# Kernel tuning notes

Measured on AMD Instinct MI355X. Metric: run time of the kernel, lower is better.

The kernel has to match this reference:

```python
import jax, jax.numpy as jnp
import numpy as np

N_HEADS = 16
D_KV = 64
TRIL_DIAG = -999999  # faithful to torch.tril(scores, diagonal=-999999)


def setup_inputs() -> dict:
    key = jax.random.key(0)
    ks = jax.random.split(key, 5)
    B, S, D = 2, 2048, 1024
    inner = N_HEADS * D_KV
    return {
        "hidden_states": jax.random.normal(ks[0], (B, S, D), dtype=jnp.float32),
        "Wq": jax.random.normal(ks[1], (inner, D), dtype=jnp.float32) * 0.02,
        "Wk": jax.random.normal(ks[2], (inner, D), dtype=jnp.float32) * 0.02,
        "Wv": jax.random.normal(ks[3], (inner, D), dtype=jnp.float32) * 0.02,
        "Wo": jax.random.normal(ks[4], (D, inner), dtype=jnp.float32) * 0.02,
    }


def reference(hidden_states, Wq, Wk, Wv, Wo):
    B, S, D = hidden_states.shape

    def shape(x):  # [B,S,inner] -> [B,H,S,Dk]
        return x.reshape(B, S, N_HEADS, D_KV).transpose(0, 2, 1, 3)

    q = shape(hidden_states @ Wq.T)
    k = shape(hidden_states @ Wk.T)
    v = shape(hidden_states @ Wv.T)

    scores = jnp.einsum("bhqd,bhkd->bhqk", q, k)  # no 1/sqrt(d) scaling, as in source
    scores = jnp.tril(scores, k=TRIL_DIAG)  # zeroes everything for S < 999999 (faithful)
    attn = jax.nn.softmax(scores.astype(jnp.float32), axis=-1).astype(scores.dtype)
    # dropout is identity at inference
    ctx = jnp.einsum("bhqk,bhkd->bhqd", attn, v)
    ctx = ctx.transpose(0, 2, 1, 3).reshape(B, S, N_HEADS * D_KV)
    return ctx @ Wo.T
```

## Files before the change

kernel.cpp:

```cpp
#include <hip/hip_runtime.h>

#define BB 2
#define SS 2048
#define DD 1024
#define INNER 1024
#define NCHUNK 64
#define ROWS_PER_CHUNK (SS / NCHUNK)

__global__ void colsum_kernel(const float* __restrict__ h, float* __restrict__ hbar) {
    int b = blockIdx.x / NCHUNK;
    int chunk = blockIdx.x % NCHUNK;
    int t = threadIdx.x;
    const float4* hp = reinterpret_cast<const float4*>(h + (size_t)b * SS * DD);
    float4 acc = make_float4(0.f, 0.f, 0.f, 0.f);
    int s0 = chunk * ROWS_PER_CHUNK;
    #pragma unroll 4
    for (int s = s0; s < s0 + ROWS_PER_CHUNK; ++s) {
        float4 v = hp[(size_t)s * (DD / 4) + t];
        acc.x += v.x; acc.y += v.y; acc.z += v.z; acc.w += v.w;
    }
    float* dst = hbar + b * DD + t * 4;
    atomicAdd(dst + 0, acc.x);
    atomicAdd(dst + 1, acc.y);
    atomicAdd(dst + 2, acc.z);
    atomicAdd(dst + 3, acc.w);
}

__global__ void matvec_kernel(const float* __restrict__ W, const float* __restrict__ x,
                              float* __restrict__ y, float scale) {
    int wave = (blockIdx.x * blockDim.x + threadIdx.x) >> 6;
    int lane = threadIdx.x & 63;
    int b = wave / INNER;
    int i = wave % INNER;
    const float4* Wp = reinterpret_cast<const float4*>(W + (size_t)i * 1024);
    const float4* xp = reinterpret_cast<const float4*>(x + b * 1024);
    float sum = 0.f;
    #pragma unroll
    for (int k4 = lane; k4 < 256; k4 += 64) {
        float4 w = Wp[k4];
        float4 xv = xp[k4];
        sum += w.x * xv.x + w.y * xv.y + w.z * xv.z + w.w * xv.w;
    }
    #pragma unroll
    for (int off = 32; off > 0; off >>= 1) sum += __shfl_down(sum, off);
    if (lane == 0) y[wave] = sum * scale;
}

__global__ void bcast_kernel(const float* __restrict__ row, float* __restrict__ out) {
    const float4* r4 = reinterpret_cast<const float4*>(row);
    float4* o4 = reinterpret_cast<float4*>(out);
    const int total4 = BB * SS * (DD / 4);
    for (int i = blockIdx.x * blockDim.x + threadIdx.x; i < total4;
         i += gridDim.x * blockDim.x) {
        int d4 = i & (DD / 4 - 1);
        int b = i >> 19;
        o4[i] = r4[b * (DD / 4) + d4];
    }
}

extern "C" void kernel_launch(void* const* d_in, const int* in_sizes, int n_in,
                              void* d_out, int out_size, void* d_ws, size_t ws_size,
                              hipStream_t stream) {
    const float* h  = (const float*)d_in[0];
    const float* Wv = (const float*)d_in[3];
    const float* Wo = (const float*)d_in[4];
    float* out = (float*)d_out;

    float* hbar  = (float*)d_ws;
    float* vmean = hbar + BB * DD;
    float* orow  = vmean + BB * INNER;

    hipMemsetAsync(hbar, 0, BB * DD * sizeof(float), stream);
    colsum_kernel<<<BB * NCHUNK, 256, 0, stream>>>(h, hbar);
    matvec_kernel<<<512, 256, 0, stream>>>(Wv, hbar, vmean, 1.0f / (float)SS);
    matvec_kernel<<<512, 256, 0, stream>>>(Wo, vmean, orow, 1.0f);
    bcast_kernel<<<2048, 256, 0, stream>>>(orow, out);
}
```

Measured before the change: 96.36 us.

## Fuse colsum, matvecs and broadcast into one cooperative kernel with grid syncs

Replaces the memset plus four separate launches with a single cooperative kernel that runs column sums, the two matvecs and the output broadcast as phases separated by grid.sync. Atomic accumulation is replaced by per-block partial sums that are reduced in a second phase. The aim is to remove launch overhead and the gaps between kernels. In exchange it adds four grid-wide barriers, limits the grid to 256 blocks, and the reduction phase runs on only 2048 threads.

Measured after the change: 209.4 us. 117% more time.

```diff
diff --git a/kernel.cpp b/kernel.cpp
--- a/kernel.cpp
+++ b/kernel.cpp
@@ -1,60 +1,109 @@
 #include <hip/hip_runtime.h>
+#include <hip/hip_cooperative_groups.h>
+
+namespace cg = cooperative_groups;
 
 #define BB 2
 #define SS 2048
 #define DD 1024
-#define INNER 1024
-#define NCHUNK 64
-#define ROWS_PER_CHUNK (SS / NCHUNK)
+#define NBLK 256
+#define NTHR 256
+#define ROWS_PER_BLK 16
 
-__global__ void colsum_kernel(const float* __restrict__ h, float* __restrict__ hbar) {
-    int b = blockIdx.x / NCHUNK;
-    int chunk = blockIdx.x % NCHUNK;
-    int t = threadIdx.x;
-    const float4* hp = reinterpret_cast<const float4*>(h + (size_t)b * SS * DD);
-    float4 acc = make_float4(0.f, 0.f, 0.f, 0.f);
-    int s0 = chunk * ROWS_PER_CHUNK;
-    #pragma unroll 4
-    for (int s = s0; s < s0 + ROWS_PER_CHUNK; ++s) {
-        float4 v = hp[(size_t)s * (DD / 4) + t];
-        acc.x += v.x; acc.y += v.y; acc.z += v.z; acc.w += v.w;
+__global__ void __launch_bounds__(NTHR, 1)
+fused_kernel(const float* __restrict__ h, const float* __restrict__ Wv,
+             const float* __restrict__ Wo, float* __restrict__ out,
+             float* __restrict__ ws) {
+    cg::grid_group grid = cg::this_grid();
+
+    float* partial = ws;
+    float* hbar    = ws + NBLK * DD;
+    float* vmean   = hbar + BB * DD;
+    float* orow    = vmean + BB * DD;
+
+    const int bid = blockIdx.x;
+    const int tid = threadIdx.x;
+    const int gtid = bid * NTHR + tid;
+    const int lane = tid & 63;
+    const int wave = gtid >> 6;
+
+    {
+        const float4* hp = reinterpret_cast<const float4*>(h);
+        float4 acc = make_float4(0.f, 0.f, 0.f, 0.f);
+        int r0 = bid * ROWS_PER_BLK;
+        #pragma unroll 4
+        for (int r = r0; r < r0 + ROWS_PER_BLK; ++r) {
+            float4 v = hp[(size_t)r * (DD / 4) + tid];
+            acc.x += v.x; acc.y += v.y; acc.z += v.z; acc.w += v.w;
+        }
+        reinterpret_cast<float4*>(partial)[bid * (DD / 4) + tid] = acc;
     }
-    float* dst = hbar + b * DD + t * 4;
-    atomicAdd(dst + 0, acc.x);
-    atomicAdd(dst + 1, acc.y);
-    atomicAdd(dst + 2, acc.z);
-    atomicAdd(dst + 3, acc.w);
-}
+    grid.sync();
 
-__global__ void matvec_kernel(const float* __restrict__ W, const float* __restrict__ x,
-                              float* __restrict__ y, float scale) {
-    int wave = (blockIdx.x * blockDim.x + threadIdx.x) >> 6;
-    int lane = threadIdx.x & 63;
-    int b = wave / INNER;
-    int i = wave % INNER;
-    const float4* Wp = reinterpret_cast<const float4*>(W + (size_t)i * 1024);
-    const float4* xp = reinterpret_cast<const float4*>(x + b * 1024);
-    float sum = 0.f;
-    #pragma unroll
-    for (int k4 = lane; k4 < 256; k4 += 64) {
-        float4 w = Wp[k4];
-        float4 xv = xp[k4];
-        sum += w.x * xv.x + w.y * xv.y + w.z * xv.z + w.w * xv.w;
+    if (gtid < BB * DD) {
+        int b = gtid >> 10;
+        int d = gtid & (DD - 1);
+        float s = 0.f;
+        #pragma unroll 8
+        for (int j = 0; j < 128; ++j)
+            s += partial[(size_t)(b * 128 + j) * DD + d];
+        hbar[gtid] = s;
     }
-    #pragma unroll
-    for (int off = 32; off > 0; off >>= 1) sum += __shfl_down(sum, off);
-    if (lane == 0) y[wave] = sum * scale;
-}
+    grid.sync();
 
-__global__ void bcast_kernel(const float* __restrict__ row, float* __restrict__ out) {
-    const float4* r4 = reinterpret_cast<const float4*>(row);
-    float4* o4 = reinterpret_cast<float4*>(out);
-    const int total4 = BB * SS * (DD / 4);
-    for (int i = blockIdx.x * blockDim.x + threadIdx.x; i < total4;
-         i += gridDim.x * blockDim.x) {
-        int d4 = i & (DD / 4 - 1);
-        int b = i >> 19;
-        o4[i] = r4[b * (DD / 4) + d4];
+    {
+        #pragma unroll
+        for (int rep = 0; rep < 2; ++rep) {
+            int o = wave + rep * 1024;
+            int b = o >> 10;
+            int i = o & (DD - 1);
+            const float4* Wp = reinterpret_cast<const float4*>(Wv + (size_t)i * DD);
+            const float4* xp = reinterpret_cast<const float4*>(hbar + b * DD);
+            float sum = 0.f;
+            #pragma unroll
+            for (int k4 = lane; k4 < DD / 4; k4 += 64) {
+                float4 w = Wp[k4];
+                float4 x = xp[k4];
+                sum += w.x * x.x + w.y * x.y + w.z * x.z + w.w * x.w;
+            }
+            #pragma unroll
+            for (int off = 32; off > 0; off >>= 1) sum += __shfl_down(sum, off);
+            if (lane == 0) vmean[o] = sum * (1.0f / (float)SS);
+        }
+    }
+    grid.sync();
+
+    {
+        #pragma unroll
+        for (int rep = 0; rep < 2; ++rep) {
+            int o = wave + rep * 1024;
+            int b = o >> 10;
+            int i = o & (DD - 1);
+            const float4* Wp = reinterpret_cast<const float4*>(Wo + (size_t)i * DD);
+            const float4* xp = reinterpret_cast<const float4*>(vmean + b * DD);
+            float sum = 0.f;
+            #pragma unroll
+            for (int k4 = lane; k4 < DD / 4; k4 += 64) {
+                float4 w = Wp[k4];
+                float4 x = xp[k4];
+                sum += w.x * x.x + w.y * x.y + w.z * x.z + w.w * x.w;
+            }
+            #pragma unroll
+            for (int off = 32; off > 0; off >>= 1) sum += __shfl_down(sum, off);
+            if (lane == 0) orow[o] = sum;
+        }
+    }
+    grid.sync();
+
+    {
+        const float4* r4 = reinterpret_cast<const float4*>(orow);
+        float4* o4 = reinterpret_cast<float4*>(out);
+        const int total4 = BB * SS * (DD / 4);
+        for (int i = gtid; i < total4; i += NBLK * NTHR) {
+            int d4 = i & (DD / 4 - 1);
+            int b = i >> 19;
+            o4[i] = r4[b * (DD / 4) + d4];
+        }
     }
 }
 
@@ -65,14 +114,9 @@
     const float* Wv = (const float*)d_in[3];
     const float* Wo = (const float*)d_in[4];
     float* out = (float*)d_out;
+    float* ws  = (float*)d_ws;
 
-    float* hbar  = (float*)d_ws;
-    float* vmean = hbar + BB * DD;
-    float* orow  = vmean + BB * INNER;
-
-    hipMemsetAsync(hbar, 0, BB * DD * sizeof(float), stream);
-    colsum_kernel<<<BB * NCHUNK, 256, 0, stream>>>(h, hbar);
-    matvec_kernel<<<512, 256, 0, stream>>>(Wv, hbar, vmean, 1.0f / (float)SS);
-    matvec_kernel<<<512, 256, 0, stream>>>(Wo, vmean, orow, 1.0f);
-    bcast_kernel<<<2048, 256, 0, stream>>>(orow, out);
+    void* args[] = { (void*)&h, (void*)&Wv, (void*)&Wo, (void*)&out, (void*)&ws };
+    hipLaunchCooperativeKernel((const void*)fused_kernel, dim3(NBLK), dim3(NTHR),
+                               args, 0, stream);
 }
```

## Replace atomics with partial sums and fuse matvecs with reduction and broadcast

Applied to the files above, without the earlier changes.

Column sums now go to per-chunk partial buffers instead of atomics, removing the memset. The first matvec reduces the partials itself into shared memory. The second matvec is fused with the output broadcast, so each block computes its own slice of the output row and writes its tile. This removes two launches but makes every block recompute the partial reduction and the Wo rows, so far more redundant reads go through L2.

After: 115.5 us. +19.9%, slower.

```diff
diff --git a/kernel.cpp b/kernel.cpp
--- a/kernel.cpp
+++ b/kernel.cpp
@@ -3,58 +3,114 @@
 #define BB 2
 #define SS 2048
 #define DD 1024
-#define INNER 1024
-#define NCHUNK 64
-#define ROWS_PER_CHUNK (SS / NCHUNK)
 
-__global__ void colsum_kernel(const float* __restrict__ h, float* __restrict__ hbar) {
-    int b = blockIdx.x / NCHUNK;
-    int chunk = blockIdx.x % NCHUNK;
+__global__ void colsum_kernel(const float* __restrict__ h, float* __restrict__ partial) {
+    int bid = blockIdx.x;
+    int b = bid >> 6;
+    int chunk = bid & 63;
     int t = threadIdx.x;
-    const float4* hp = reinterpret_cast<const float4*>(h + (size_t)b * SS * DD);
+    const float4* hp = reinterpret_cast<const float4*>(h) + (size_t)b * SS * (DD / 4);
     float4 acc = make_float4(0.f, 0.f, 0.f, 0.f);
-    int s0 = chunk * ROWS_PER_CHUNK;
+    int s0 = chunk * 32;
     #pragma unroll 4
-    for (int s = s0; s < s0 + ROWS_PER_CHUNK; ++s) {
+    for (int s = s0; s < s0 + 32; ++s) {
         float4 v = hp[(size_t)s * (DD / 4) + t];
         acc.x += v.x; acc.y += v.y; acc.z += v.z; acc.w += v.w;
     }
-    float* dst = hbar + b * DD + t * 4;
-    atomicAdd(dst + 0, acc.x);
-    atomicAdd(dst + 1, acc.y);
-    atomicAdd(dst + 2, acc.z);
-    atomicAdd(dst + 3, acc.w);
+    reinterpret_cast<float4*>(partial)[(size_t)bid * (DD / 4) + t] = acc;
 }
 
-__global__ void matvec_kernel(const float* __restrict__ W, const float* __restrict__ x,
-                              float* __restrict__ y, float scale) {
-    int wave = (blockIdx.x * blockDim.x + threadIdx.x) >> 6;
-    int lane = threadIdx.x & 63;
-    int b = wave / INNER;
-    int i = wave % INNER;
-    const float4* Wp = reinterpret_cast<const float4*>(W + (size_t)i * 1024);
-    const float4* xp = reinterpret_cast<const float4*>(x + b * 1024);
-    float sum = 0.f;
+__global__ void matvec1_kernel(const float* __restrict__ Wv, const float* __restrict__ partial,
+                               float* __restrict__ vmean) {
+    __shared__ float4 hbar4[2 * (DD / 4)];
+    int t = threadIdx.x;
+    const float4* p4 = reinterpret_cast<const float4*>(partial);
+    float4 a0 = make_float4(0.f, 0.f, 0.f, 0.f);
+    float4 a1 = make_float4(0.f, 0.f, 0.f, 0.f);
+    #pragma unroll 8
+    for (int j = 0; j < 64; ++j) {
+        float4 v0 = p4[(size_t)j * (DD / 4) + t];
+        float4 v1 = p4[(size_t)(64 + j) * (DD / 4) + t];
+        a0.x += v0.x; a0.y += v0.y; a0.z += v0.z; a0.w += v0.w;
+        a1.x += v1.x; a1.y += v1.y; a1.z += v1.z; a1.w += v1.w;
+    }
+    hbar4[t] = a0;
+    hbar4[256 + t] = a1;
+    __syncthreads();
+
+    int wv = t >> 6, lane = t & 63;
+    int i0 = blockIdx.x * 32;
     #pragma unroll
-    for (int k4 = lane; k4 < 256; k4 += 64) {
-        float4 w = Wp[k4];
-        float4 xv = xp[k4];
-        sum += w.x * xv.x + w.y * xv.y + w.z * xv.z + w.w * xv.w;
+    for (int r = 0; r < 16; ++r) {
+        int ol = wv * 16 + r;
+        int il = ol >> 1, b = ol & 1;
+        int i = i0 + il;
+        const float4* Wp = reinterpret_cast<const float4*>(Wv) + (size_t)i * (DD / 4);
+        float sum = 0.f;
+        #pragma unroll
+        for (int p = 0; p < 4; ++p) {
+            float4 w = Wp[lane + p * 64];
+            float4 x = hbar4[b * 256 + lane + p * 64];
+            sum += w.x * x.x + w.y * x.y + w.z * x.z + w.w * x.w;
+        }
+        #pragma unroll
+        for (int off = 32; off > 0; off >>= 1) sum += __shfl_down(sum, off);
+        if (lane == 0) vmean[b * DD + i] = sum * (1.0f / (float)SS);
     }
-    #pragma unroll
-    for (int off = 32; off > 0; off >>= 1) sum += __shfl_down(sum, off);
-    if (lane == 0) y[wave] = sum * scale;
 }
 
-__global__ void bcast_kernel(const float* __restrict__ row, float* __restrict__ out) {
-    const float4* r4 = reinterpret_cast<const float4*>(row);
+__global__ void matvec2_bcast_kernel(const float* __restrict__ Wo, const float* __restrict__ vmean,
+                                     float* __restrict__ out) {
+    __shared__ float4 vm4[2 * (DD / 4)];
+    __shared__ float4 orow4[2 * 32];
+    int t = threadIdx.x, wv = t >> 6, lane = t & 63;
+    int bid = blockIdx.x;
+    int sc = bid >> 3, ic = bid & 7;
+    int i0 = ic * 128, s0 = sc * 128;
+
+    const float4* vg = reinterpret_cast<const float4*>(vmean);
+    vm4[t] = vg[t];
+    vm4[256 + t] = vg[256 + t];
+    __syncthreads();
+
+    float4 x0[4], x1[4];
+    #pragma unroll
+    for (int p = 0; p < 4; ++p) {
+        x0[p] = vm4[lane + p * 64];
+        x1[p] = vm4[256 + lane + p * 64];
+    }
+
+    float* orow = reinterpret_cast<float*>(orow4);
+    #pragma unroll 4
+    for (int r = 0; r < 32; ++r) {
+        int il = wv * 32 + r;
+        int i = i0 + il;
+        const float4* Wp = reinterpret_cast<const float4*>(Wo) + (size_t)i * (DD / 4);
+        float sb0 = 0.f, sb1 = 0.f;
+        #pragma unroll
+        for (int p = 0; p < 4; ++p) {
+            float4 w = Wp[lane + p * 64];
+            sb0 += w.x * x0[p].x + w.y * x0[p].y + w.z * x0[p].z + w.w * x0[p].w;
+            sb1 += w.x * x1[p].x + w.y * x1[p].y + w.z * x1[p].z + w.w * x1[p].w;
+        }
+        #pragma unroll
+        for (int off = 32; off > 0; off >>= 1) {
+            sb0 += __shfl_down(sb0, off);
+            sb1 += __shfl_down(sb1, off);
+        }
+        if (lane == 0) {
+            orow[0 * 128 + il] = sb0;
+            orow[1 * 128 + il] = sb1;
+        }
+    }
+    __syncthreads();
+
     float4* o4 = reinterpret_cast<float4*>(out);
-    const int total4 = BB * SS * (DD / 4);
-    for (int i = blockIdx.x * blockDim.x + threadIdx.x; i < total4;
-         i += gridDim.x * blockDim.x) {
-        int d4 = i & (DD / 4 - 1);
-        int b = i >> 19;
-        o4[i] = r4[b * (DD / 4) + d4];
+    for (int j = t; j < 8192; j += 256) {
+        int q4 = j & 31;
+        int s = (j >> 5) & 127;
+        int b = j >> 12;
+        o4[((size_t)(b * SS + s0 + s)) * (DD / 4) + ic * 32 + q4] = orow4[b * 32 + q4];
     }
 }
 
@@ -66,13 +122,10 @@
     const float* Wo = (const float*)d_in[4];
     float* out = (float*)d_out;
 
-    float* hbar  = (float*)d_ws;
-    float* vmean = hbar + BB * DD;
-    float* orow  = vmean + BB * INNER;
+    float* partial = (float*)d_ws;
+    float* vmean   = partial + 128 * DD;
 
-    hipMemsetAsync(hbar, 0, BB * DD * sizeof(float), stream);
-    colsum_kernel<<<BB * NCHUNK, 256, 0, stream>>>(h, hbar);
-    matvec_kernel<<<512, 256, 0, stream>>>(Wv, hbar, vmean, 1.0f / (float)SS);
-    matvec_kernel<<<512, 256, 0, stream>>>(Wo, vmean, orow, 1.0f);
-    bcast_kernel<<<2048, 256, 0, stream>>>(orow, out);
+    colsum_kernel<<<128, 256, 0, stream>>>(h, partial);
+    matvec1_kernel<<<32, 256, 0, stream>>>(Wv, partial, vmean);
+    matvec2_bcast_kernel<<<128, 256, 0, stream>>>(Wo, vmean, out);
 }
```
